# Kernel optimization log

Hardware: AMD Instinct MI355X
Metric: run time of the kernel (lower is better)

Reference implementation:

```python
import jax, jax.numpy as jnp
import numpy as np


def setup_inputs() -> dict:
    key = jax.random.key(0)
    k1, k2, k3, k4, k5 = jax.random.split(key, 5)
    M, K, N, E = 16384, 2048, 5632, 8  # total_tokens, d_model, expert ffn dim, num_experts
    a = jax.random.normal(k1, (M, K), jnp.float32) * 0.1          # fp8-valued activations (simulated in f32)
    b = jax.random.normal(k2, (E, N, K), jnp.float32) * 0.05      # column-major expert weights [E, N, K]
    scale_a = jax.random.uniform(k3, (M, 1), jnp.float32, 0.5, 1.5)   # per-token dequant scale
    scale_b = jax.random.uniform(k4, (E, 1), jnp.float32, 0.5, 1.5)   # per-expert dequant scale
    cuts = jnp.sort(jax.random.randint(k5, (E - 1,), 0, M)).astype(jnp.int32)
    seg_indptr = jnp.concatenate([jnp.zeros(1, jnp.int32), cuts, jnp.full((1,), M, jnp.int32)])
    return {"a": a, "b": b, "scale_a": scale_a, "scale_b": scale_b,
            "seg_indptr": seg_indptr, "batch_size": E}


def reference(a, b, scale_a, scale_b, seg_indptr, batch_size):
    # Grouped GEMM: for expert e, rows seg_indptr[e]:seg_indptr[e+1] of `a` are
    # multiplied by b[e]^T (b is column-major [E, N, K]).
    M = a.shape[0]
    E = b.shape[0]
    group_sizes = jnp.diff(seg_indptr).astype(jnp.int32)           # [E]
    out = jax.lax.ragged_dot(a, jnp.swapaxes(b, 1, 2), group_sizes)  # [M, N]
    # fp8 w8a8 dequant: per-token scale_a, per-expert scale_b gathered per token
    eid = jnp.clip(jnp.searchsorted(seg_indptr, jnp.arange(M), side='right') - 1, 0, E - 1)
    return out * scale_a * scale_b[eid]
```

## Files before the change

kernel.cpp:

```cpp
#include <hip/hip_runtime.h>


#define KSLICE 32
#define NSLICE 64
#define BM 256
#define BN 256

typedef __attribute__((ext_vector_type(4))) float f32x4;
typedef __attribute__((ext_vector_type(4))) unsigned int u32x4;
using frag_ab = __attribute__((ext_vector_type(8))) short;
using frag_cd = __attribute__((ext_vector_type(4))) float;

__device__ __forceinline__ unsigned int pack_bf2(float x, float y) {
  unsigned int ux = __float_as_uint(x);
  unsigned int uy = __float_as_uint(y);
  ux += 0x7fffu + ((ux >> 16) & 1u);
  uy += 0x7fffu + ((uy >> 16) & 1u);
  return (ux >> 16) | (uy & 0xffff0000u);
}

__device__ __forceinline__ void gload_lds16(const void* g, void* lds) {
  __builtin_amdgcn_global_load_lds(
      (const __attribute__((address_space(1))) unsigned int*)g,
      (__attribute__((address_space(3))) unsigned int*)lds, 16, 0, 0);
}

__global__ __launch_bounds__(256)
void convert_kernel(const float* __restrict__ A, const float* __restrict__ B,
                    unsigned short* __restrict__ wa, unsigned short* __restrict__ wb) {
  constexpr long long NA = 16384LL * 2048;
  constexpr long long NB = 8LL * 5632 * 2048;
  constexpr long long NA8 = NA / 8;
  constexpr long long NTOT = (NA + NB) / 8;
  for (long long c = (long long)blockIdx.x * 256 + threadIdx.x; c < NTOT;
       c += (long long)gridDim.x * 256) {
    const float* src;
    unsigned short* dst;
    long long off;
    if (c < NA8) { src = A; dst = wa; off = c * 8; }
    else         { src = B; dst = wb; off = (c - NA8) * 8; }
    f32x4 v0 = *(const f32x4*)(src + off);
    f32x4 v1 = *(const f32x4*)(src + off + 4);
    u32x4 o;
    o[0] = pack_bf2(v0[0], v0[1]);
    o[1] = pack_bf2(v0[2], v0[3]);
    o[2] = pack_bf2(v1[0], v1[1]);
    o[3] = pack_bf2(v1[2], v1[3]);
    *(u32x4*)(dst + off) = o;
  }
}

__global__ __launch_bounds__(512, 2)
void ggemm8(const unsigned short* __restrict__ A,
            const unsigned short* __restrict__ B,
            const float* __restrict__ sa,
            const float* __restrict__ sb,
            const int* __restrict__ seg,
            float* __restrict__ C) {
  constexpr int M = 16384, K = 2048, N = 5632, E = 8;
  constexpr int NT = N / BN;
  const int nwg = (M / BM) * NT;

  int bid = blockIdx.x;
  int sid = (bid & 7) * (nwg >> 3) + (bid >> 3);
  int mt = sid / NT, nt = sid % NT;
  int m0 = mt * BM, n0 = nt * BN;

  int tid = threadIdx.x;
  int lane = tid & 63;
  int w = tid >> 6;
  int wrow = (w >> 2) * 128;
  int wcol = (w & 3) * 64;
  int l16 = lane & 15, lhi = lane >> 4;

  __shared__ unsigned short Alds[4 * 8192];
  __shared__ unsigned short Blds[4 * 8192];

  int rpl = lane >> 3;
  int slog = (lane & 7) ^ rpl;
  int srow = rpl * 2 + (slog >> 2);
  int sk0 = (slog & 3) * 8;
  const unsigned short* gA0 = A + (size_t)(m0 + w * 32 + srow) * K + sk0;
  const unsigned short* gA1 = gA0 + (size_t)16 * K;
  unsigned short* ldsA0 = &Alds[(w * 2 + 0) * 512];
  unsigned short* ldsA1 = &Alds[(w * 2 + 1) * 512];
  unsigned short* ldsB0 = &Blds[(w * 2 + 0) * 512];
  unsigned short* ldsB1 = &Blds[(w * 2 + 1) * 512];

  int offA[8], offB[4];
#pragma unroll
  for (int i = 0; i < 8; ++i) {
    int r = wrow + i * 16 + l16;
    int rp = r >> 1;
    int sl = ((r & 1) << 2) | lhi;
    offA[i] = rp * 64 + ((sl ^ (rp & 7)) << 3);
  }
#pragma unroll
  for (int j = 0; j < 4; ++j) {
    int r = wcol + j * 16 + l16;
    int rp = r >> 1;
    int sl = ((r & 1) << 2) | lhi;
    offB[j] = rp * 64 + ((sl ^ (rp & 7)) << 3);
  }

  for (int e = 0; e < E; ++e) {
    int rlo = max(m0, seg[e]);
    int rhi = min(m0 + BM, seg[e + 1]);
    if (rlo >= rhi) continue;

    const unsigned short* gB0 =
        B + (size_t)e * N * K + (size_t)(n0 + w * 32 + srow) * K + sk0;
    const unsigned short* gB1 = gB0 + (size_t)16 * K;

    frag_cd acc[8][4];
#pragma unroll
    for (int i = 0; i < 8; ++i)
#pragma unroll
      for (int j = 0; j < 4; ++j) acc[i][j] = (frag_cd){0.f, 0.f, 0.f, 0.f};

    auto stage = [&](int s) {
      int slot = (s & 3) * 8192;
      int g = s * KSLICE;
      gload_lds16(gA0 + g, ldsA0 + slot);
      gload_lds16(gA1 + g, ldsA1 + slot);
      gload_lds16(gB0 + g, ldsB0 + slot);
      gload_lds16(gB1 + g, ldsB1 + slot);
    };

    auto phase = [&](int s, auto vmwait) {
      int slot = (s & 3) * 8192;
      frag_ab af[8], bf[4];
#pragma unroll
      for (int i = 0; i < 8; ++i)
        af[i] = *(const frag_ab*)(&Alds[slot + offA[i]]);
#pragma unroll
      for (int j = 0; j < 4; ++j)
        bf[j] = *(const frag_ab*)(&Blds[slot + offB[j]]);
      if (s + 3 < NSLICE) stage(s + 3);
      vmwait();
      __builtin_amdgcn_s_barrier();
      asm volatile("s_waitcnt lgkmcnt(0)" ::: "memory");
      __builtin_amdgcn_s_setprio(1);
#pragma unroll
      for (int i = 0; i < 8; ++i)
#pragma unroll
        for (int j = 0; j < 4; ++j)
          acc[i][j] = __builtin_amdgcn_mfma_f32_16x16x32_bf16(
              af[i], bf[j], acc[i][j], 0, 0, 0);
      __builtin_amdgcn_s_setprio(0);
      __builtin_amdgcn_s_barrier();
    };

    auto W8 = [] { asm volatile("s_waitcnt vmcnt(8)" ::: "memory"); };
    auto W4 = [] { asm volatile("s_waitcnt vmcnt(4)" ::: "memory"); };
    auto W0 = [] { asm volatile("s_waitcnt vmcnt(0)" ::: "memory"); };

    stage(0); stage(1); stage(2);
    asm volatile("s_waitcnt vmcnt(8)" ::: "memory");
    __builtin_amdgcn_s_barrier();

#pragma unroll 4
    for (int s = 0; s < NSLICE - 4; ++s) phase(s, W8);
    phase(NSLICE - 4, W8);
    phase(NSLICE - 3, W4);
    phase(NSLICE - 2, W0);
    phase(NSLICE - 1, W0);

    float sbe = sb[e];
#pragma unroll
    for (int i = 0; i < 8; ++i) {
#pragma unroll
      for (int r = 0; r < 4; ++r) {
        int grow = m0 + wrow + i * 16 + lhi * 4 + r;
        if (grow >= rlo && grow < rhi) {
          float s = sa[grow] * sbe;
          float* Crow = C + (size_t)grow * N + n0 + wcol;
#pragma unroll
          for (int j = 0; j < 4; ++j)
            Crow[j * 16 + l16] = acc[i][j][r] * s;
        }
      }
    }
  }
}

extern "C" void kernel_launch(void* const* d_in, const int* in_sizes, int n_in,
                              void* d_out, int out_size, void* d_ws, size_t ws_size,
                              hipStream_t stream) {
  const float* a = (const float*)d_in[0];
  const float* b = (const float*)d_in[1];
  const float* sa = (const float*)d_in[2];
  const float* sb = (const float*)d_in[3];
  const int* seg = (const int*)d_in[4];
  float* out = (float*)d_out;

  constexpr size_t NA = 16384ULL * 2048;
  constexpr size_t NB = 8ULL * 5632 * 2048;
  unsigned short* wa = (unsigned short*)d_ws;
  unsigned short* wb = wa + NA;

  hipLaunchKernelGGL(convert_kernel, dim3(2048), dim3(256), 0, stream, a, b, wa, wb);
  hipLaunchKernelGGL(ggemm8, dim3((16384 / BM) * (5632 / BN)), dim3(512), 0, stream,
                     wa, wb, sa, sb, seg, out);
}
```

Baseline: 790.2 us.

## Restructure grouped GEMM mainloop into quadrant-pipelined BK=64 double-buffered schedule

Replaces the 4-slot, 32-wide K pipeline with a 2-buffer, 64-wide K tile split into four 128x128 quadrants. Each wave computes a 64x32 subtile per quadrant, and global-to-LDS loads for tile t+2 are interleaved between the quadrant MFMA groups with barriers in between. The aim is to overlap memory traffic with MFMA work at finer granularity and to reuse A/B fragments across quadrants, cutting LDS reads per MFMA. The cost is more barriers per tile and a more intricate buffer-reuse order, which could introduce stalls or races if the wait counts are wrong.

```diff
diff --git a/kernel.cpp b/kernel.cpp
--- a/kernel.cpp
+++ b/kernel.cpp
@@ -1,10 +1,11 @@
 #include <hip/hip_runtime.h>
 
 
-#define KSLICE 32
-#define NSLICE 64
+#define BK 64
+#define NTILES 32
 #define BM 256
 #define BN 256
+#define KDIM 2048
 
 typedef __attribute__((ext_vector_type(4))) float f32x4;
 typedef __attribute__((ext_vector_type(4))) unsigned int u32x4;
@@ -51,133 +52,149 @@
 }
 
 __global__ __launch_bounds__(512, 2)
-void ggemm8(const unsigned short* __restrict__ A,
-            const unsigned short* __restrict__ B,
-            const float* __restrict__ sa,
-            const float* __restrict__ sb,
-            const int* __restrict__ seg,
-            float* __restrict__ C) {
-  constexpr int M = 16384, K = 2048, N = 5632, E = 8;
-  constexpr int NT = N / BN;
-  const int nwg = (M / BM) * NT;
+void ggemm_q(const unsigned short* __restrict__ A,
+             const unsigned short* __restrict__ B,
+             const float* __restrict__ sa,
+             const float* __restrict__ sb,
+             const int* __restrict__ seg,
+             float* __restrict__ C) {
+  constexpr int M = 16384, N = 5632, E = 8;
+  constexpr int NTC = N / BN;
+  const int nwg = (M / BM) * NTC;
 
   int bid = blockIdx.x;
   int sid = (bid & 7) * (nwg >> 3) + (bid >> 3);
-  int mt = sid / NT, nt = sid % NT;
+  int mt = sid / NTC, nt = sid % NTC;
   int m0 = mt * BM, n0 = nt * BN;
 
-  int tid = threadIdx.x;
-  int lane = tid & 63;
-  int w = tid >> 6;
-  int wrow = (w >> 2) * 128;
-  int wcol = (w & 3) * 64;
+  int tid = threadIdx.x, lane = tid & 63, w = tid >> 6;
   int l16 = lane & 15, lhi = lane >> 4;
-
-  __shared__ unsigned short Alds[4 * 8192];
-  __shared__ unsigned short Blds[4 * 8192];
-
-  int rpl = lane >> 3;
-  int slog = (lane & 7) ^ rpl;
-  int srow = rpl * 2 + (slog >> 2);
-  int sk0 = (slog & 3) * 8;
-  const unsigned short* gA0 = A + (size_t)(m0 + w * 32 + srow) * K + sk0;
-  const unsigned short* gA1 = gA0 + (size_t)16 * K;
-  unsigned short* ldsA0 = &Alds[(w * 2 + 0) * 512];
-  unsigned short* ldsA1 = &Alds[(w * 2 + 1) * 512];
-  unsigned short* ldsB0 = &Blds[(w * 2 + 0) * 512];
-  unsigned short* ldsB1 = &Blds[(w * 2 + 1) * 512];
-
-  int offA[8], offB[4];
-#pragma unroll
-  for (int i = 0; i < 8; ++i) {
-    int r = wrow + i * 16 + l16;
-    int rp = r >> 1;
-    int sl = ((r & 1) << 2) | lhi;
-    offA[i] = rp * 64 + ((sl ^ (rp & 7)) << 3);
-  }
-#pragma unroll
-  for (int j = 0; j < 4; ++j) {
-    int r = wcol + j * 16 + l16;
-    int rp = r >> 1;
-    int sl = ((r & 1) << 2) | lhi;
-    offB[j] = rp * 64 + ((sl ^ (rp & 7)) << 3);
-  }
+  int rw = (w & 1) * 64;
+  int cw = (w >> 1) * 32;
+
+  __shared__ unsigned short lds[2][2][2][8192];
+
+  int c7 = l16 & 7;
+  int x0 = (lhi ^ c7) * 8;
+  int x1 = ((4 | lhi) ^ c7) * 8;
+  int offA = (rw + l16) * 64;
+  int offB = (cw + l16) * 64;
+  int srow = lane >> 3;
+  int scol = ((lane & 7) ^ srow) * 8;
+
+  const unsigned short* gA = A + (size_t)(m0 + w * 16 + srow) * KDIM + scol;
+
+  frag_ab af[2][4], bf0[2][2], bf1[2][2];
 
   for (int e = 0; e < E; ++e) {
     int rlo = max(m0, seg[e]);
     int rhi = min(m0 + BM, seg[e + 1]);
     if (rlo >= rhi) continue;
-
-    const unsigned short* gB0 =
-        B + (size_t)e * N * K + (size_t)(n0 + w * 32 + srow) * K + sk0;
-    const unsigned short* gB1 = gB0 + (size_t)16 * K;
-
-    frag_cd acc[8][4];
-#pragma unroll
-    for (int i = 0; i < 8; ++i)
-#pragma unroll
-      for (int j = 0; j < 4; ++j) acc[i][j] = (frag_cd){0.f, 0.f, 0.f, 0.f};
-
-    auto stage = [&](int s) {
-      int slot = (s & 3) * 8192;
-      int g = s * KSLICE;
-      gload_lds16(gA0 + g, ldsA0 + slot);
-      gload_lds16(gA1 + g, ldsA1 + slot);
-      gload_lds16(gB0 + g, ldsB0 + slot);
-      gload_lds16(gB1 + g, ldsB1 + slot);
-    };
-
-    auto phase = [&](int s, auto vmwait) {
-      int slot = (s & 3) * 8192;
-      frag_ab af[8], bf[4];
-#pragma unroll
-      for (int i = 0; i < 8; ++i)
-        af[i] = *(const frag_ab*)(&Alds[slot + offA[i]]);
-#pragma unroll
-      for (int j = 0; j < 4; ++j)
-        bf[j] = *(const frag_ab*)(&Blds[slot + offB[j]]);
-      if (s + 3 < NSLICE) stage(s + 3);
-      vmwait();
-      __builtin_amdgcn_s_barrier();
-      asm volatile("s_waitcnt lgkmcnt(0)" ::: "memory");
+    const unsigned short* gB =
+        B + (size_t)e * N * KDIM + (size_t)(n0 + w * 16 + srow) * KDIM + scol;
+
+    frag_cd acc[4][4][2];
+#pragma unroll
+    for (int qi = 0; qi < 4; ++qi)
+#pragma unroll
+      for (int f = 0; f < 4; ++f)
+#pragma unroll
+        for (int g = 0; g < 2; ++g) acc[qi][f][g] = (frag_cd){0.f, 0.f, 0.f, 0.f};
+
+    auto stA = [&](int buf, int half, int t) {
+#pragma unroll
+      for (int i = 0; i < 2; ++i)
+        gload_lds16(gA + (size_t)(half * 128 + i * 8) * KDIM + t * BK,
+                    &lds[buf][0][half][(w * 16 + i * 8) * 64]);
+    };
+    auto stB = [&](int buf, int half, int t) {
+#pragma unroll
+      for (int i = 0; i < 2; ++i)
+        gload_lds16(gB + (size_t)(half * 128 + i * 8) * KDIM + t * BK,
+                    &lds[buf][1][half][(w * 16 + i * 8) * 64]);
+    };
+    auto rdAf = [&](int buf, int half) {
+      const unsigned short* p = &lds[buf][0][half][0];
+#pragma unroll
+      for (int f = 0; f < 4; ++f) {
+        af[0][f] = *(const frag_ab*)(p + offA + f * 1024 + x0);
+        af[1][f] = *(const frag_ab*)(p + offA + f * 1024 + x1);
+      }
+    };
+    auto rdBf = [&](int buf, int half, frag_ab (&bf)[2][2]) {
+      const unsigned short* p = &lds[buf][1][half][0];
+#pragma unroll
+      for (int g = 0; g < 2; ++g) {
+        bf[0][g] = *(const frag_ab*)(p + offB + g * 1024 + x0);
+        bf[1][g] = *(const frag_ab*)(p + offB + g * 1024 + x1);
+      }
+    };
+    auto mfma16 = [&](int qi, frag_ab (&bf)[2][2]) {
       __builtin_amdgcn_s_setprio(1);
 #pragma unroll
-      for (int i = 0; i < 8; ++i)
-#pragma unroll
-        for (int j = 0; j < 4; ++j)
-          acc[i][j] = __builtin_amdgcn_mfma_f32_16x16x32_bf16(
-              af[i], bf[j], acc[i][j], 0, 0, 0);
+      for (int f = 0; f < 4; ++f)
+#pragma unroll
+        for (int g = 0; g < 2; ++g)
+#pragma unroll
+          for (int ks = 0; ks < 2; ++ks)
+            acc[qi][f][g] = __builtin_amdgcn_mfma_f32_16x16x32_bf16(
+                af[ks][f], bf[ks][g], acc[qi][f][g], 0, 0, 0);
       __builtin_amdgcn_s_setprio(0);
-      __builtin_amdgcn_s_barrier();
-    };
-
-    auto W8 = [] { asm volatile("s_waitcnt vmcnt(8)" ::: "memory"); };
-    auto W4 = [] { asm volatile("s_waitcnt vmcnt(4)" ::: "memory"); };
-    auto W0 = [] { asm volatile("s_waitcnt vmcnt(0)" ::: "memory"); };
-
-    stage(0); stage(1); stage(2);
+    };
+
+    stA(0, 0, 0); stB(0, 0, 0); stB(0, 1, 0); stA(0, 1, 0);
+    stA(1, 0, 1); stB(1, 0, 1); stB(1, 1, 1); stA(1, 1, 1);
     asm volatile("s_waitcnt vmcnt(8)" ::: "memory");
     __builtin_amdgcn_s_barrier();
 
-#pragma unroll 4
-    for (int s = 0; s < NSLICE - 4; ++s) phase(s, W8);
-    phase(NSLICE - 4, W8);
-    phase(NSLICE - 3, W4);
-    phase(NSLICE - 2, W0);
-    phase(NSLICE - 1, W0);
-
+    auto tile_body = [&](int t, int buf) {
+      bool st = (t + 2 < NTILES);
+      rdAf(buf, 0);
+      rdBf(buf, 0, bf0);
+      __builtin_amdgcn_s_barrier();
+      mfma16(0, bf0);
+      rdBf(buf, 1, bf1);
+      if (st) { stA(buf, 0, t + 2); stB(buf, 0, t + 2); }
+      __builtin_amdgcn_s_barrier();
+      mfma16(1, bf1);
+      rdAf(buf, 1);
+      if (st) stB(buf, 1, t + 2);
+      __builtin_amdgcn_s_barrier();
+      mfma16(2, bf1);
+      if (st) stA(buf, 1, t + 2);
+      if (t < NTILES - 2) {
+        asm volatile("s_waitcnt vmcnt(8)" ::: "memory");
+      } else if (t == NTILES - 2) {
+        asm volatile("s_waitcnt vmcnt(0)" ::: "memory");
+      }
+      __builtin_amdgcn_s_barrier();
+      mfma16(3, bf0);
+    };
+
+    for (int t2 = 0; t2 < NTILES; t2 += 2) {
+      tile_body(t2, 0);
+      tile_body(t2 + 1, 1);
+    }
+
+    const int QMAP[4] = {0, 2, 3, 1};
     float sbe = sb[e];
 #pragma unroll
-    for (int i = 0; i < 8; ++i) {
-#pragma unroll
-      for (int r = 0; r < 4; ++r) {
-        int grow = m0 + wrow + i * 16 + lhi * 4 + r;
-        if (grow >= rlo && grow < rhi) {
-          float s = sa[grow] * sbe;
-          float* Crow = C + (size_t)grow * N + n0 + wcol;
-#pragma unroll
-          for (int j = 0; j < 4; ++j)
-            Crow[j * 16 + l16] = acc[i][j][r] * s;
+    for (int qi = 0; qi < 4; ++qi) {
+      int q = QMAP[qi];
+      int rbase = m0 + (q & 1) * 128 + rw;
+      int cbase = n0 + (q >> 1) * 128 + cw;
+#pragma unroll
+      for (int f = 0; f < 4; ++f) {
+#pragma unroll
+        for (int r = 0; r < 4; ++r) {
+          int grow = rbase + f * 16 + lhi * 4 + r;
+          if (grow >= rlo && grow < rhi) {
+            float s = sa[grow] * sbe;
+            float* Crow = C + (size_t)grow * N + cbase;
+#pragma unroll
+            for (int g = 0; g < 2; ++g)
+              Crow[g * 16 + l16] = acc[qi][f][g][r] * s;
+          }
         }
       }
     }
@@ -195,11 +212,10 @@
   float* out = (float*)d_out;
 
   constexpr size_t NA = 16384ULL * 2048;
-  constexpr size_t NB = 8ULL * 5632 * 2048;
   unsigned short* wa = (unsigned short*)d_ws;
   unsigned short* wb = wa + NA;
 
   hipLaunchKernelGGL(convert_kernel, dim3(2048), dim3(256), 0, stream, a, b, wa, wb);
-  hipLaunchKernelGGL(ggemm8, dim3((16384 / BM) * (5632 / BN)), dim3(512), 0, stream,
+  hipLaunchKernelGGL(ggemm_q, dim3((16384 / BM) * (5632 / BN)), dim3(512), 0, stream,
                      wa, wb, sa, sb, seg, out);
 }
```

New measurement: 757.6 us. 4.1% less time.
